# Kernel optimization log

Measured on AMD Instinct MI355X. Metric: run time of the kernel, lower is better.

Reference implementation:

```python
import jax, jax.numpy as jnp
import numpy as np

DT = 0.1  # CFG.dt from original code (Euler step size)
B, T, L = 16, 2000, 1024


def setup_inputs() -> dict:
    key = jax.random.key(0)
    z = jax.random.normal(key, (B, T, L), dtype=jnp.float32)
    return {"z": z}


def _fh_forward(z):
    b, t, l = z.shape
    v0 = jnp.zeros((b, l), dtype=z.dtype)
    s0 = jnp.zeros((b, l), dtype=z.dtype)

    def step(carry, z_k):
        v, s = carry
        # FitzHugh-Nagumo Euler update (matches V[:,k] and S[:,k] in torch)
        v_new = (1.0 + DT) * v - (DT / 3.0) * v ** 3 - DT * s + DT * z_k
        s_new = s + DT * 0.08 * (v + 0.7 - 0.8 * s)
        return (v_new, s_new), v_new

    # V[:,k] depends on z[:,k-1], k = 1..T-1; V[:,0] = 0
    zs = jnp.swapaxes(z[:, : t - 1, :], 0, 1)  # (T-1, B, L)
    _, vs = jax.lax.scan(step, (v0, s0), zs)    # vs: (T-1, B, L)
    V = jnp.concatenate([v0[None], vs], axis=0)  # (T, B, L)
    return jnp.swapaxes(V, 0, 1) / 2.0           # (B, T, L)


def reference(z):
    return _fh_forward(z)
```

## Files before the change

kernel.cpp:

```cpp
#include <hip/hip_runtime.h>

#define T_STEPS 2000
#define B_DIM 16
#define L_DIM 1024

__device__ __forceinline__ float vmulf(float a, float b) {
    float d; asm("v_mul_f32 %0, %1, %2" : "=v"(d) : "v"(a), "v"(b)); return d;
}
__device__ __forceinline__ float vaddf(float a, float b) {
    float d; asm("v_add_f32 %0, %1, %2" : "=v"(d) : "v"(a), "v"(b)); return d;
}
__device__ __forceinline__ float vfma(float a, float b, float c) {
    float d; asm("v_fma_f32 %0, %1, %2, %3" : "=v"(d) : "v"(a), "v"(b), "v"(c)); return d;
}
__device__ __forceinline__ float vfma_negc(float a, float b, float c) {
    float d; asm("v_fma_f32 %0, %1, %2, -%3" : "=v"(d) : "v"(a), "v"(b), "v"(c)); return d;
}
__device__ __forceinline__ float vfma_nega(float a, float b, float c) {
    float d; asm("v_fma_f32 %0, -%1, %2, %3" : "=v"(d) : "v"(a), "v"(b), "v"(c)); return d;
}

__global__ __launch_bounds__(64, 1) void fh_kernel(const float* __restrict__ z,
                                                   float* __restrict__ out) {
    const float C_1P = (float)(1.0 + 0.1);
    const float C_3  = (float)(0.1 / 3.0);
    const float C_DT = 0.1f;
    const float C_SK = (float)(0.1 * 0.08);
    const float C_07 = 0.7f;
    const float C_08 = 0.8f;

    const int idx = blockIdx.x * 64 + threadIdx.x;
    const int b = idx >> 10;
    const int l = idx & 1023;
    const size_t base = (size_t)b * T_STEPS * L_DIM + l;
    const float* zp = z + base;
    float* outp = out + base;

    constexpr int STEPS = T_STEPS - 1;
    constexpr int D = 64;
    constexpr int SAFE = 1920;
    constexpr int TAIL = STEPS - 1984;

    float v = 0.0f, s = 0.0f;

    outp[0] = 0.0f;
    outp += L_DIM;

    float ring[D];
#pragma unroll
    for (int i = 0; i < D; ++i)
        ring[i] = zp[(size_t)i * L_DIM];

#define FH_STEP(ZK)                                            \
    do {                                                       \
        const float v3 = vmulf(vmulf(v, v), v);                \
        const float t2 = vmulf(C_3, v3);                       \
        const float a1 = vfma_negc(C_1P, v, t2);               \
        const float a2 = vfma_nega(C_DT, s, a1);               \
        const float vn = vfma(C_DT, (ZK), a2);                 \
        const float u1 = vaddf(v, C_07);                       \
        const float u3 = vfma_nega(C_08, s, u1);               \
        s = vfma(C_SK, u3, s);                                 \
        v = vn;                                                \
        __builtin_nontemporal_store(vmulf(0.5f, v), outp);     \
        outp += L_DIM;                                         \
    } while (0)

    for (int c = 0; c < SAFE; c += D) {
        const float* zpf = zp + (size_t)(c + D) * L_DIM;
#pragma unroll
        for (int i = 0; i < D; ++i) {
            const float zk = ring[i];
            ring[i] = zpf[(size_t)i * L_DIM];
            FH_STEP(zk);
        }
    }

    {
        const float* zpf = zp + (size_t)(SAFE + D) * L_DIM;
#pragma unroll
        for (int i = 0; i < D; ++i) {
            const float zk = ring[i];
            const int io = (i < TAIL) ? i : (TAIL - 1);
            ring[i] = zpf[(size_t)io * L_DIM];
            FH_STEP(zk);
        }
    }

#pragma unroll
    for (int i = 0; i < TAIL; ++i) {
        const float zk = ring[i];
        FH_STEP(zk);
    }
#undef FH_STEP
}

extern "C" void kernel_launch(void* const* d_in, const int* in_sizes, int n_in,
                              void* d_out, int out_size, void* d_ws, size_t ws_size,
                              hipStream_t stream) {
    const float* z = (const float*)d_in[0];
    float* out = (float*)d_out;
    const int total = B_DIM * L_DIM;
    dim3 grid(total / 64);
    dim3 block(64);
    hipLaunchKernelGGL(fh_kernel, grid, block, 0, stream, z, out);
}
```

Baseline: 84.63 us.

## Split compute and store into separate waves with double-buffered LDS

Each block now has two waves. Wave 0 runs the serial FitzHugh-Nagumo recurrence and writes each 64-step chunk of outputs into a double-buffered LDS array. Wave 1 drains the previous chunk from LDS to global memory with nontemporal stores. The z prefetch changes from an interleaved ring to ping-pong register rings that are filled in bulk before each chunk. The aim is to take global store issue off the latency-bound recurrence path. The cost is a block barrier per chunk that keeps the two waves in lockstep, plus extra LDS traffic.

```diff
diff --git a/kernel.cpp b/kernel.cpp
--- a/kernel.cpp
+++ b/kernel.cpp
@@ -20,8 +20,8 @@
     float d; asm("v_fma_f32 %0, -%1, %2, %3" : "=v"(d) : "v"(a), "v"(b), "v"(c)); return d;
 }
 
-__global__ __launch_bounds__(64, 1) void fh_kernel(const float* __restrict__ z,
-                                                   float* __restrict__ out) {
+__global__ __launch_bounds__(128, 1) void fh_kernel(const float* __restrict__ z,
+                                                    float* __restrict__ out) {
     const float C_1P = (float)(1.0 + 0.1);
     const float C_3  = (float)(0.1 / 3.0);
     const float C_DT = 0.1f;
@@ -29,70 +29,91 @@
     const float C_07 = 0.7f;
     const float C_08 = 0.8f;
 
-    const int idx = blockIdx.x * 64 + threadIdx.x;
+    __shared__ float vbuf[2][64][64];
+
+    const int wv = threadIdx.x >> 6;
+    const int lane = threadIdx.x & 63;
+    const int idx = blockIdx.x * 64 + lane;
     const int b = idx >> 10;
     const int l = idx & 1023;
     const size_t base = (size_t)b * T_STEPS * L_DIM + l;
-    const float* zp = z + base;
-    float* outp = out + base;
 
-    constexpr int STEPS = T_STEPS - 1;
-    constexpr int D = 64;
-    constexpr int SAFE = 1920;
-    constexpr int TAIL = STEPS - 1984;
+    if (wv == 0) {
+        const float* zp = z + base;
+        float v = 0.0f, s = 0.0f;
+        float ringA[64], ringB[64];
 
-    float v = 0.0f, s = 0.0f;
+#pragma unroll
+        for (int i = 0; i < 64; ++i)
+            ringA[i] = zp[(size_t)i * L_DIM];
 
-    outp[0] = 0.0f;
-    outp += L_DIM;
+#define FH_STEP(ZK, P, I)                                    \
+        do {                                                 \
+            const float v3 = vmulf(vmulf(v, v), v);          \
+            const float t2 = vmulf(C_3, v3);                 \
+            const float a1 = vfma_negc(C_1P, v, t2);         \
+            const float a2 = vfma_nega(C_DT, s, a1);         \
+            const float vn = vfma(C_DT, (ZK), a2);           \
+            const float u1 = vaddf(v, C_07);                 \
+            const float u3 = vfma_nega(C_08, s, u1);         \
+            s = vfma(C_SK, u3, s);                           \
+            v = vn;                                          \
+            vbuf[P][I][lane] = vmulf(0.5f, v);               \
+        } while (0)
 
-    float ring[D];
+        for (int pp = 0; pp < 15; ++pp) {
+            {
+                const float* zpf = zp + (size_t)(2 * pp * 64 + 64) * L_DIM;
 #pragma unroll
-    for (int i = 0; i < D; ++i)
-        ring[i] = zp[(size_t)i * L_DIM];
-
-#define FH_STEP(ZK)                                            \
-    do {                                                       \
-        const float v3 = vmulf(vmulf(v, v), v);                \
-        const float t2 = vmulf(C_3, v3);                       \
-        const float a1 = vfma_negc(C_1P, v, t2);               \
-        const float a2 = vfma_nega(C_DT, s, a1);               \
-        const float vn = vfma(C_DT, (ZK), a2);                 \
-        const float u1 = vaddf(v, C_07);                       \
-        const float u3 = vfma_nega(C_08, s, u1);               \
-        s = vfma(C_SK, u3, s);                                 \
-        v = vn;                                                \
-        __builtin_nontemporal_store(vmulf(0.5f, v), outp);     \
-        outp += L_DIM;                                         \
-    } while (0)
-
-    for (int c = 0; c < SAFE; c += D) {
-        const float* zpf = zp + (size_t)(c + D) * L_DIM;
+                for (int i = 0; i < 64; ++i) ringB[i] = zpf[(size_t)i * L_DIM];
 #pragma unroll
-        for (int i = 0; i < D; ++i) {
-            const float zk = ring[i];
-            ring[i] = zpf[(size_t)i * L_DIM];
-            FH_STEP(zk);
+                for (int i = 0; i < 64; ++i) { const float zk = ringA[i]; FH_STEP(zk, 0, i); }
+                __syncthreads();
+            }
+            {
+                const float* zpf = zp + (size_t)((2 * pp + 1) * 64 + 64) * L_DIM;
+#pragma unroll
+                for (int i = 0; i < 64; ++i) ringA[i] = zpf[(size_t)i * L_DIM];
+#pragma unroll
+                for (int i = 0; i < 64; ++i) { const float zk = ringB[i]; FH_STEP(zk, 1, i); }
+                __syncthreads();
+            }
+        }
+        {
+            const float* zpf = zp + (size_t)1984 * L_DIM;
+#pragma unroll
+            for (int i = 0; i < 64; ++i) {
+                const int io = (i < 15) ? i : 14;
+                ringB[i] = zpf[(size_t)io * L_DIM];
+            }
+#pragma unroll
+            for (int i = 0; i < 64; ++i) { const float zk = ringA[i]; FH_STEP(zk, 0, i); }
+            __syncthreads();
+        }
+        {
+#pragma unroll
+            for (int i = 0; i < 15; ++i) { const float zk = ringB[i]; FH_STEP(zk, 1, i); }
+            __syncthreads();
+        }
+        __syncthreads();
+#undef FH_STEP
+    } else {
+        float* outp = out + base;
+        __builtin_nontemporal_store(0.0f, outp);
+        __syncthreads();
+        for (int ph = 1; ph <= 32; ++ph) {
+            const int c = ph - 1;
+            const int len = (c == 31) ? 15 : 64;
+            const int buf = c & 1;
+            float* op = outp + (size_t)(c * 64 + 1) * L_DIM;
+            for (int i = 0; i < len; ++i) {
+                const float val = vbuf[buf][i][lane];
+                __builtin_nontemporal_store(val, op);
+                op += L_DIM;
+            }
+            __syncthreads();
         }
     }
-
-    {
-        const float* zpf = zp + (size_t)(SAFE + D) * L_DIM;
-#pragma unroll
-        for (int i = 0; i < D; ++i) {
-            const float zk = ring[i];
-            const int io = (i < TAIL) ? i : (TAIL - 1);
-            ring[i] = zpf[(size_t)io * L_DIM];
-            FH_STEP(zk);
-        }
-    }
-
-#pragma unroll
-    for (int i = 0; i < TAIL; ++i) {
-        const float zk = ring[i];
-        FH_STEP(zk);
-    }
-#undef FH_STEP
 }
 
 extern "C" void kernel_launch(void* const* d_in, const int* in_sizes, int n_in,
@@ -100,8 +121,7 @@
                               hipStream_t stream) {
     const float* z = (const float*)d_in[0];
     float* out = (float*)d_out;
-    const int total = B_DIM * L_DIM;
-    dim3 grid(total / 64);
-    dim3 block(64);
+    dim3 grid(256);
+    dim3 block(128);
     hipLaunchKernelGGL(fh_kernel, grid, block, 0, stream, z, out);
 }
```

After: 85.81 us. Within noise of the previous version (+1.4%).
